# Optimization experiments

Measured on AMD Instinct MI355X. Metric: run time of the kernel, lower is better.

## Reference

```python
import jax, jax.numpy as jnp
import numpy as np

NUM_LAYERS = 2

def setup_inputs() -> dict:
    key = jax.random.key(0)
    ks = jax.random.split(key, 10)
    N, E, V, D, G = 50000, 800000, 100000, 128, 64
    node_ids = jax.random.randint(ks[0], (N,), 0, V)
    edge_index = jax.random.randint(ks[1], (2, E), 0, N)
    batch = jnp.sort(jax.random.randint(ks[2], (N,), 0, G))
    embed = jax.random.normal(ks[3], (V, D), dtype=jnp.float32)
    conv_w = jax.random.normal(ks[4], (NUM_LAYERS, D, D), dtype=jnp.float32) * (1.0 / np.sqrt(D))
    w_ih = jax.random.normal(ks[5], (3 * D, D), dtype=jnp.float32) * (1.0 / np.sqrt(D))
    w_hh = jax.random.normal(ks[6], (3 * D, D), dtype=jnp.float32) * (1.0 / np.sqrt(D))
    b_ih = jax.random.normal(ks[7], (3 * D,), dtype=jnp.float32) * 0.01
    b_hh = jax.random.normal(ks[8], (3 * D,), dtype=jnp.float32) * 0.01
    return {"node_ids": node_ids, "edge_index": edge_index, "batch": batch,
            "num_graphs": 64, "embed": embed, "conv_w": conv_w,
            "w_ih": w_ih, "w_hh": w_hh, "b_ih": b_ih, "b_hh": b_hh}


def _gru_cell(x, h, w_ih, w_hh, b_ih, b_hh):
    # torch.nn.GRUCell math; gate order r, z, n
    gi = x @ w_ih.T + b_ih
    gh = h @ w_hh.T + b_hh
    i_r, i_z, i_n = jnp.split(gi, 3, axis=-1)
    h_r, h_z, h_n = jnp.split(gh, 3, axis=-1)
    r = jax.nn.sigmoid(i_r + h_r)
    z = jax.nn.sigmoid(i_z + h_z)
    n = jnp.tanh(i_n + r * h_n)
    return (1.0 - z) * n + z * h


def reference(node_ids, edge_index, batch, num_graphs, embed, conv_w, w_ih, w_hh, b_ih, b_hh):
    N = node_ids.shape[0]
    src, dst = edge_index[0], edge_index[1]
    h = embed[node_ids]  # [N, D]
    for i in range(NUM_LAYERS):
        m = h @ conv_w[i]                                   # [N, D]
        agg = jax.ops.segment_sum(m[src], dst, num_segments=N)  # scatter-add messages
        h = _gru_cell(agg, h, w_ih, w_hh, b_ih, b_hh)
    # global mean pool per graph
    sums = jax.ops.segment_sum(h, batch, num_segments=num_graphs)       # [G, D]
    counts = jax.ops.segment_sum(jnp.ones((N,), h.dtype), batch, num_segments=num_graphs)
    return sums / jnp.maximum(counts, 1.0)[:, None]
```

## Files before the change

kernel.cpp:

```cpp
#include <hip/hip_runtime.h>
#include <hip/hip_bf16.h>


#define DTHREADS 256
#define BSHIFT 7
#define BNODES 128

typedef __attribute__((ext_vector_type(8))) short bf16x8;
typedef __attribute__((ext_vector_type(4))) float f32x4;

__device__ __forceinline__ float sigf(float x) { return 1.0f / (1.0f + __expf(-x)); }
__device__ __forceinline__ float tanhfast(float x) { return 1.0f - 2.0f / (1.0f + __expf(2.0f * x)); }

__device__ __forceinline__ unsigned short f2bf_rne(float x) {
  unsigned int u = __float_as_uint(x);
  u += 0x7fff + ((u >> 16) & 1);
  return (unsigned short)(u >> 16);
}
__device__ __forceinline__ float bf2f(unsigned int lo16) {
  return __uint_as_float(lo16 << 16);
}

__global__ __launch_bounds__(DTHREADS) void gather_kernel(
    const float* __restrict__ embed, const int* __restrict__ node_ids,
    unsigned short* __restrict__ hb, int N) {
  int idx = blockIdx.x * DTHREADS + threadIdx.x;
  if (idx >= N * 32) return;
  int n = idx >> 5;
  int c = (idx & 31) * 4;
  int v = node_ids[n];
  float4 val = *(const float4*)&embed[(size_t)v * 128 + c];
  unsigned short b[4] = {f2bf_rne(val.x), f2bf_rne(val.y), f2bf_rne(val.z), f2bf_rne(val.w)};
  *(ushort4*)&hb[(size_t)n * 128 + c] = *(ushort4*)b;
}

__global__ __launch_bounds__(DTHREADS) void bucket_hist_kernel(
    const int* __restrict__ dst, int* __restrict__ gcnt, int E, int NB) {
  __shared__ int lc[512];
  int tid = threadIdx.x;
  for (int i = tid; i < NB; i += DTHREADS) lc[i] = 0;
  __syncthreads();
  int base = blockIdx.x * 4096;
  #pragma unroll
  for (int q = 0; q < 16; ++q) {
    int e = base + q * 256 + tid;
    if (e < E) atomicAdd(&lc[dst[e] >> BSHIFT], 1);
  }
  __syncthreads();
  for (int i = tid; i < NB; i += DTHREADS) {
    int c = lc[i];
    if (c) atomicAdd(&gcnt[i], c);
  }
}

__global__ __launch_bounds__(512) void bucket_scan_kernel(
    const int* __restrict__ gcnt, int* __restrict__ ptr, int* __restrict__ cur,
    int* __restrict__ row_ptr, int NB, int N) {
  int tid = threadIdx.x;
  int lane = tid & 63, wv = tid >> 6;
  int v = (tid < NB) ? gcnt[tid] : 0;
  int x = v;
  #pragma unroll
  for (int off = 1; off < 64; off <<= 1) {
    int y = __shfl_up(x, (unsigned)off, 64);
    if (lane >= off) x += y;
  }
  __shared__ int ws[8];
  if (lane == 63) ws[wv] = x;
  __syncthreads();
  int woff = 0;
  for (int w = 0; w < wv; ++w) woff += ws[w];
  int excl = woff + x - v;
  if (tid < NB) { ptr[tid] = excl; cur[tid] = excl; }
  if (tid == 511) { int tot = woff + x; ptr[NB] = tot; row_ptr[N] = tot; }
}

__global__ __launch_bounds__(DTHREADS) void bucket_scatter_kernel(
    const int* __restrict__ src, const int* __restrict__ dst,
    int* __restrict__ cur, unsigned int* __restrict__ ebuf, int E, int NB) {
  __shared__ int lc[512];
  __shared__ int lbs[512];
  int tid = threadIdx.x;
  for (int i = tid; i < NB; i += DTHREADS) lc[i] = 0;
  __syncthreads();
  int base = blockIdx.x * 4096;
  int rank[16];
  #pragma unroll
  for (int q = 0; q < 16; ++q) {
    int e = base + q * 256 + tid;
    if (e < E) rank[q] = atomicAdd(&lc[dst[e] >> BSHIFT], 1);
  }
  __syncthreads();
  for (int i = tid; i < NB; i += DTHREADS) {
    int c = lc[i];
    lbs[i] = c ? atomicAdd(&cur[i], c) : 0;
  }
  __syncthreads();
  #pragma unroll
  for (int q = 0; q < 16; ++q) {
    int e = base + q * 256 + tid;
    if (e < E) {
      int d = dst[e];
      unsigned int pk = (unsigned int)src[e] | ((unsigned int)(d & (BNODES - 1)) << 17);
      ebuf[lbs[d >> BSHIFT] + rank[q]] = pk;
    }
  }
}

__global__ __launch_bounds__(DTHREADS) void bucket_sort_kernel(
    const unsigned int* __restrict__ ebuf, const int* __restrict__ ptr,
    int* __restrict__ row_ptr, int* __restrict__ csr_src, int N) {
  __shared__ int cnt[BNODES];
  __shared__ int sc[BNODES];
  const int tid = threadIdx.x;
  const int b = blockIdx.x;
  const int s = ptr[b], e = ptr[b + 1];
  if (tid < BNODES) cnt[tid] = 0;
  __syncthreads();
  for (int i = s + tid; i < e; i += DTHREADS)
    atomicAdd(&cnt[ebuf[i] >> 17], 1);
  __syncthreads();
  if (tid < BNODES) sc[tid] = cnt[tid];
  __syncthreads();
  #pragma unroll
  for (int off = 1; off < BNODES; off <<= 1) {
    int t = 0;
    if (tid < BNODES && tid >= off) t = sc[tid - off];
    __syncthreads();
    if (tid < BNODES) sc[tid] += t;
    __syncthreads();
  }
  if (tid < BNODES) {
    int excl = sc[tid] - cnt[tid];
    int n = b * BNODES + tid;
    if (n < N) row_ptr[n] = s + excl;
    cnt[tid] = excl;
  }
  __syncthreads();
  for (int i = s + tid; i < e; i += DTHREADS) {
    unsigned int pk = ebuf[i];
    int slot = atomicAdd(&cnt[pk >> 17], 1);
    csr_src[s + slot] = (int)(pk & 0x1FFFFu);
  }
}

__global__ __launch_bounds__(DTHREADS) void pack_w_kernel(
    const float* __restrict__ w, unsigned short* __restrict__ wpk, int J) {
  int f = blockIdx.x * DTHREADS + threadIdx.x;
  if (f >= J * 16) return;
  int l = f & 63;
  int s = (f >> 6) & 3;
  int t = (f >> 8) & 3;
  int jb = f >> 10;
  int j = jb * 64 + t * 16 + (l & 15);
  int kb = s * 32 + (l >> 4) * 8;
  unsigned short o[8];
  #pragma unroll
  for (int i = 0; i < 8; ++i) o[i] = f2bf_rne(w[j * 128 + kb + i]);
  *(uint4*)&wpk[(size_t)f * 8] = *(uint4*)o;
}

__global__ __launch_bounds__(DTHREADS) void pack_wc_kernel(
    const float* __restrict__ conv, const float* __restrict__ w_ih,
    unsigned short* __restrict__ wpk) {
  int id = blockIdx.x * DTHREADS + threadIdx.x;
  if (id >= 384 * 128) return;
  int f = id >> 3, i = id & 7;
  int l = f & 63;
  int s = (f >> 6) & 3;
  int t = (f >> 8) & 3;
  int jb = f >> 10;
  int j = jb * 64 + t * 16 + (l & 15);
  int k = s * 32 + (l >> 4) * 8 + i;
  float acc = 0.f;
  for (int d = 0; d < 128; d += 4) {
    float4 cv = *(const float4*)&conv[k * 128 + d];
    float4 wv = *(const float4*)&w_ih[j * 128 + d];
    acc += cv.x * wv.x + cv.y * wv.y + cv.z * wv.z + cv.w * wv.w;
  }
  wpk[(size_t)f * 8 + i] = f2bf_rne(acc);
}

__global__ __launch_bounds__(DTHREADS) void aggregate_kernel(
    const unsigned short* __restrict__ hb, const int* __restrict__ row_ptr,
    const int* __restrict__ csr_src, unsigned short* __restrict__ agg, int N) {
  int w = (blockIdx.x * DTHREADS + threadIdx.x) >> 6;
  if (w >= N) return;
  int lane = threadIdx.x & 63;
  int g = lane >> 4;
  int c = lane & 15;
  int s = row_ptr[w], e = row_ptr[w + 1];
  float acc[8] = {0.f, 0.f, 0.f, 0.f, 0.f, 0.f, 0.f, 0.f};
  for (int i = s; i < e; i += 8) {
    int iA = i + g, iB = i + g + 4;
    bool vA = iA < e, vB = iB < e;
    int sA = csr_src[vA ? iA : s];
    int sB = csr_src[vB ? iB : s];
    uint4 a = *(const uint4*)&hb[(size_t)sA * 128 + c * 8];
    uint4 b = *(const uint4*)&hb[(size_t)sB * 128 + c * 8];
    const unsigned int* ap = (const unsigned int*)&a;
    const unsigned int* bp = (const unsigned int*)&b;
    if (vA) {
      #pragma unroll
      for (int q = 0; q < 4; ++q) {
        acc[2 * q]     += bf2f(ap[q] & 0xffffu);
        acc[2 * q + 1] += bf2f(ap[q] >> 16);
      }
    }
    if (vB) {
      #pragma unroll
      for (int q = 0; q < 4; ++q) {
        acc[2 * q]     += bf2f(bp[q] & 0xffffu);
        acc[2 * q + 1] += bf2f(bp[q] >> 16);
      }
    }
  }
  #pragma unroll
  for (int q = 0; q < 8; ++q) acc[q] += __shfl_xor(acc[q], 16, 64);
  #pragma unroll
  for (int q = 0; q < 8; ++q) acc[q] += __shfl_xor(acc[q], 32, 64);
  if (g == 0) {
    unsigned int o[4];
    #pragma unroll
    for (int q = 0; q < 4; ++q)
      o[q] = (unsigned int)f2bf_rne(acc[2 * q]) | ((unsigned int)f2bf_rne(acc[2 * q + 1]) << 16);
    *(uint4*)&agg[(size_t)w * 128 + c * 8] = *(uint4*)o;
  }
}

__global__ __launch_bounds__(DTHREADS) void fused_gru_kernel(
    const unsigned short* __restrict__ aggb, const unsigned short* __restrict__ wpk_wc,
    const unsigned short* __restrict__ wpk_hh, const float* __restrict__ b_ih,
    const float* __restrict__ b_hh, unsigned short* __restrict__ hb, int N) {
  __shared__ __align__(16) unsigned short Ag[32 * 128];
  __shared__ __align__(16) unsigned short Hs[32 * 128];
  const int tid = threadIdx.x;
  const int n0 = blockIdx.x * 32;

  #pragma unroll
  for (int it = 0; it < 2; ++it) {
    int c = it * 256 + tid;
    int row = c >> 4, col = c & 15;
    int n = n0 + row;
    uint4 va = make_uint4(0, 0, 0, 0), vh = make_uint4(0, 0, 0, 0);
    if (n < N) {
      va = *(const uint4*)&aggb[(size_t)n * 128 + col * 8];
      vh = *(const uint4*)&hb[(size_t)n * 128 + col * 8];
    }
    int dc = col ^ (row & 15);
    *(uint4*)&Ag[row * 128 + dc * 8] = va;
    *(uint4*)&Hs[row * 128 + dc * 8] = vh;
  }
  __syncthreads();

  const int wv = tid >> 6, lane = tid & 63;
  const int lm = lane & 15, quad = lane >> 4;

  f32x4 accI[2][2][3], accH[2][2][3];
  #pragma unroll
  for (int mi = 0; mi < 2; ++mi)
    #pragma unroll
    for (int u = 0; u < 2; ++u)
      #pragma unroll
      for (int g = 0; g < 3; ++g) {
        accI[mi][u][g] = (f32x4){0.f, 0.f, 0.f, 0.f};
        accH[mi][u][g] = (f32x4){0.f, 0.f, 0.f, 0.f};
      }

  #pragma unroll
  for (int s = 0; s < 4; ++s) {
    bf16x8 afA[2], afH[2];
    #pragma unroll
    for (int mi = 0; mi < 2; ++mi) {
      int m = mi * 16 + lm;
      int chunk = (s * 4 + quad) ^ (m & 15);
      afA[mi] = *(const bf16x8*)&Ag[m * 128 + chunk * 8];
      afH[mi] = *(const bf16x8*)&Hs[m * 128 + chunk * 8];
    }
    #pragma unroll
    for (int g = 0; g < 3; ++g) {
      int jb = g * 2 + (wv >> 1);
      #pragma unroll
      for (int u = 0; u < 2; ++u) {
        int t = (wv & 1) * 2 + u;
        size_t f = ((size_t)(jb * 4 + t) * 4 + s) * 64 + lane;
        bf16x8 bI = *(const bf16x8*)&wpk_wc[f * 8];
        bf16x8 bH = *(const bf16x8*)&wpk_hh[f * 8];
        #pragma unroll
        for (int mi = 0; mi < 2; ++mi) {
          accI[mi][u][g] = __builtin_amdgcn_mfma_f32_16x16x32_bf16(afA[mi], bI, accI[mi][u][g], 0, 0, 0);
          accH[mi][u][g] = __builtin_amdgcn_mfma_f32_16x16x32_bf16(afH[mi], bH, accH[mi][u][g], 0, 0, 0);
        }
      }
    }
  }

  #pragma unroll
  for (int u = 0; u < 2; ++u) {
    int jc = wv * 32 + u * 16 + lm;
    float bir = b_ih[jc], biz = b_ih[128 + jc], bin_ = b_ih[256 + jc];
    float bhr = b_hh[jc], bhz = b_hh[128 + jc], bhn = b_hh[256 + jc];
    int c0 = jc >> 3, ej = jc & 7;
    #pragma unroll
    for (int mi = 0; mi < 2; ++mi) {
      #pragma unroll
      for (int r = 0; r < 4; ++r) {
        int row = mi * 16 + quad * 4 + r;
        int n = n0 + row;
        if (n >= N) continue;
        float ir = accI[mi][u][0][r] + bir;
        float iz = accI[mi][u][1][r] + biz;
        float in_ = accI[mi][u][2][r] + bin_;
        float hr = accH[mi][u][0][r] + bhr;
        float hz = accH[mi][u][1][r] + bhz;
        float hn = accH[mi][u][2][r] + bhn;
        float rr = sigf(ir + hr);
        float zz = sigf(iz + hz);
        float nn = tanhfast(in_ + rr * hn);
        float hold = bf2f((unsigned int)Hs[row * 128 + ((c0 ^ (row & 15)) * 8) + ej]);
        hb[(size_t)n * 128 + jc] = f2bf_rne((1.f - zz) * nn + zz * hold);
      }
    }
  }
}

__global__ __launch_bounds__(DTHREADS) void pool1_kernel(
    const unsigned short* __restrict__ hb, const int* __restrict__ batch,
    float* __restrict__ outsum, int N) {
  int b = blockIdx.x;
  int c = threadIdx.x & 127;
  int half = threadIdx.x >> 7;
  int nbeg = b * 64;
  int nend = min(nbeg + 64, N);
  float acc = 0.f;
  int cur = -1;
  for (int n = nbeg + half; n < nend; n += 2) {
    int g = batch[n];
    if (g != cur) {
      if (cur >= 0) atomicAdd(&outsum[(size_t)cur * 128 + c], acc);
      acc = 0.f;
      cur = g;
    }
    acc += bf2f((unsigned int)hb[(size_t)n * 128 + c]);
  }
  if (cur >= 0) atomicAdd(&outsum[(size_t)cur * 128 + c], acc);
}

__device__ __forceinline__ int lbound(const int* a, int n, int key) {
  int lo = 0, hi = n;
  while (lo < hi) {
    int mid = (lo + hi) >> 1;
    if (a[mid] < key) lo = mid + 1; else hi = mid;
  }
  return lo;
}

__global__ __launch_bounds__(128) void pool2_kernel(
    const float* __restrict__ outsum, const int* __restrict__ batch,
    float* __restrict__ out, int N) {
  int g = blockIdx.x;
  int c = threadIdx.x;
  int lo = lbound(batch, N, g);
  int hi = lbound(batch, N, g + 1);
  out[(size_t)g * 128 + c] = outsum[(size_t)g * 128 + c] / (float)max(hi - lo, 1);
}

extern "C" void kernel_launch(void* const* d_in, const int* in_sizes, int n_in,
                              void* d_out, int out_size, void* d_ws, size_t ws_size,
                              hipStream_t stream) {
  const int* node_ids = (const int*)d_in[0];
  const int* edge_index = (const int*)d_in[1];
  const int* batch = (const int*)d_in[2];
  const float* embed = (const float*)d_in[4];
  const float* conv_w = (const float*)d_in[5];
  const float* w_ih = (const float*)d_in[6];
  const float* w_hh = (const float*)d_in[7];
  const float* b_ih = (const float*)d_in[8];
  const float* b_hh = (const float*)d_in[9];
  float* out = (float*)d_out;

  const int N = in_sizes[0];
  const int E = in_sizes[1] / 2;
  const int G = out_size / 128;
  const int NUM_LAYERS = in_sizes[5] / (128 * 128);
  const int NB = (N + BNODES - 1) >> BSHIFT;

  const int* e_src = edge_index;
  const int* e_dst = edge_index + E;

  char* p = (char*)d_ws;
  unsigned short* hb = (unsigned short*)p;    p += (size_t)N * 128 * 2;
  unsigned short* aggb = (unsigned short*)p;  p += (size_t)N * 128 * 2;
  float* outsum = (float*)p;                  p += (size_t)G * 128 * 4;
  unsigned short* wpk_hh = (unsigned short*)p; p += (size_t)384 * 128 * 2;
  unsigned short* wpk_wc = (unsigned short*)p; p += (size_t)NUM_LAYERS * 384 * 128 * 2;
  int* bkt_cnt = (int*)p;  p += 512 * 4;
  int* bkt_ptr = (int*)p;  p += 513 * 4;
  int* bkt_cur = (int*)p;  p += 512 * 4;
  int* row_ptr = (int*)p;  p += (size_t)(N + 1) * 4;
  unsigned int* ebuf = (unsigned int*)p;  p += (size_t)E * 4;
  int* csr_src = (int*)p;  p += (size_t)E * 4;

  const int nEB = (E + 4095) / 4096;

  hipMemsetAsync(bkt_cnt, 0, 512 * sizeof(int), stream);
  hipMemsetAsync(outsum, 0, (size_t)G * 128 * sizeof(float), stream);

  bucket_hist_kernel<<<nEB, DTHREADS, 0, stream>>>(e_dst, bkt_cnt, E, NB);
  bucket_scan_kernel<<<1, 512, 0, stream>>>(bkt_cnt, bkt_ptr, bkt_cur, row_ptr, NB, N);
  bucket_scatter_kernel<<<nEB, DTHREADS, 0, stream>>>(e_src, e_dst, bkt_cur, ebuf, E, NB);
  bucket_sort_kernel<<<NB, DTHREADS, 0, stream>>>(ebuf, bkt_ptr, row_ptr, csr_src, N);

  pack_w_kernel<<<(384 * 16 + DTHREADS - 1) / DTHREADS, DTHREADS, 0, stream>>>(w_hh, wpk_hh, 384);
  for (int L = 0; L < NUM_LAYERS; ++L)
    pack_wc_kernel<<<(384 * 128 + DTHREADS - 1) / DTHREADS, DTHREADS, 0, stream>>>(
        conv_w + (size_t)L * 128 * 128, w_ih, wpk_wc + (size_t)L * 384 * 128);

  gather_kernel<<<(N * 32 + DTHREADS - 1) / DTHREADS, DTHREADS, 0, stream>>>(embed, node_ids, hb, N);

  const int nb32 = (N + 31) / 32;
  for (int L = 0; L < NUM_LAYERS; ++L) {
    aggregate_kernel<<<((size_t)N * 64 + DTHREADS - 1) / DTHREADS, DTHREADS, 0, stream>>>(
        hb, row_ptr, csr_src, aggb, N);
    fused_gru_kernel<<<nb32, DTHREADS, 0, stream>>>(
        aggb, wpk_wc + (size_t)L * 384 * 128, wpk_hh, b_ih, b_hh, hb, N);
  }

  pool1_kernel<<<(N + 63) / 64, DTHREADS, 0, stream>>>(hb, batch, outsum, N);
  pool2_kernel<<<G, 128, 0, stream>>>(outsum, batch, out, N);
}
```

Before: 327.1 us.

## Make GRU kernel persistent with register-resident weights and prefetched tiles

Turns the fused GRU kernel into a persistent kernel with 256 blocks of 512 threads. Each wave holds its slice of the packed W_ih·conv and W_hh fragments in registers for the whole run instead of reloading them per 32-node tile. The next tile's agg/h rows are prefetched into registers while the current tile is computed, at the cost of an extra barrier and high register pressure. The aggregate kernel is also unrolled to issue four neighbour gathers per lane per iteration instead of two, to raise memory-level parallelism.

```diff
diff --git a/kernel.cpp b/kernel.cpp
--- a/kernel.cpp
+++ b/kernel.cpp
@@ -3,8 +3,6 @@
 
 
 #define DTHREADS 256
-#define BSHIFT 7
-#define BNODES 128
 
 typedef __attribute__((ext_vector_type(8))) short bf16x8;
 typedef __attribute__((ext_vector_type(4))) float f32x4;
@@ -33,6 +31,9 @@
   unsigned short b[4] = {f2bf_rne(val.x), f2bf_rne(val.y), f2bf_rne(val.z), f2bf_rne(val.w)};
   *(ushort4*)&hb[(size_t)n * 128 + c] = *(ushort4*)b;
 }
+
+#define BSHIFT 7
+#define BNODES 128
 
 __global__ __launch_bounds__(DTHREADS) void bucket_hist_kernel(
     const int* __restrict__ dst, int* __restrict__ gcnt, int E, int NB) {
@@ -191,27 +192,26 @@
   int c = lane & 15;
   int s = row_ptr[w], e = row_ptr[w + 1];
   float acc[8] = {0.f, 0.f, 0.f, 0.f, 0.f, 0.f, 0.f, 0.f};
-  for (int i = s; i < e; i += 8) {
-    int iA = i + g, iB = i + g + 4;
-    bool vA = iA < e, vB = iB < e;
-    int sA = csr_src[vA ? iA : s];
-    int sB = csr_src[vB ? iB : s];
-    uint4 a = *(const uint4*)&hb[(size_t)sA * 128 + c * 8];
-    uint4 b = *(const uint4*)&hb[(size_t)sB * 128 + c * 8];
-    const unsigned int* ap = (const unsigned int*)&a;
-    const unsigned int* bp = (const unsigned int*)&b;
-    if (vA) {
-      #pragma unroll
-      for (int q = 0; q < 4; ++q) {
-        acc[2 * q]     += bf2f(ap[q] & 0xffffu);
-        acc[2 * q + 1] += bf2f(ap[q] >> 16);
-      }
-    }
-    if (vB) {
-      #pragma unroll
-      for (int q = 0; q < 4; ++q) {
-        acc[2 * q]     += bf2f(bp[q] & 0xffffu);
-        acc[2 * q + 1] += bf2f(bp[q] >> 16);
+  for (int i = s; i < e; i += 16) {
+    int idx[4]; bool vl[4]; uint4 d[4];
+    #pragma unroll
+    for (int q = 0; q < 4; ++q) {
+      int ii = i + g + q * 4;
+      vl[q] = ii < e;
+      idx[q] = csr_src[vl[q] ? ii : s];
+    }
+    #pragma unroll
+    for (int q = 0; q < 4; ++q)
+      d[q] = *(const uint4*)&hb[(size_t)idx[q] * 128 + c * 8];
+    #pragma unroll
+    for (int q = 0; q < 4; ++q) {
+      if (vl[q]) {
+        const unsigned int* dp = (const unsigned int*)&d[q];
+        #pragma unroll
+        for (int k = 0; k < 4; ++k) {
+          acc[2 * k]     += bf2f(dp[k] & 0xffffu);
+          acc[2 * k + 1] += bf2f(dp[k] >> 16);
+        }
       }
     }
   }
@@ -228,79 +228,92 @@
   }
 }
 
-__global__ __launch_bounds__(DTHREADS) void fused_gru_kernel(
+__global__ __launch_bounds__(512, 2) void fused_gru_kernel(
     const unsigned short* __restrict__ aggb, const unsigned short* __restrict__ wpk_wc,
     const unsigned short* __restrict__ wpk_hh, const float* __restrict__ b_ih,
-    const float* __restrict__ b_hh, unsigned short* __restrict__ hb, int N) {
+    const float* __restrict__ b_hh, unsigned short* __restrict__ hb,
+    int N, int nchunks) {
   __shared__ __align__(16) unsigned short Ag[32 * 128];
   __shared__ __align__(16) unsigned short Hs[32 * 128];
   const int tid = threadIdx.x;
-  const int n0 = blockIdx.x * 32;
-
-  #pragma unroll
-  for (int it = 0; it < 2; ++it) {
-    int c = it * 256 + tid;
-    int row = c >> 4, col = c & 15;
-    int n = n0 + row;
-    uint4 va = make_uint4(0, 0, 0, 0), vh = make_uint4(0, 0, 0, 0);
-    if (n < N) {
-      va = *(const uint4*)&aggb[(size_t)n * 128 + col * 8];
-      vh = *(const uint4*)&hb[(size_t)n * 128 + col * 8];
-    }
-    int dc = col ^ (row & 15);
-    *(uint4*)&Ag[row * 128 + dc * 8] = va;
-    *(uint4*)&Hs[row * 128 + dc * 8] = vh;
-  }
-  __syncthreads();
-
   const int wv = tid >> 6, lane = tid & 63;
   const int lm = lane & 15, quad = lane >> 4;
 
-  f32x4 accI[2][2][3], accH[2][2][3];
-  #pragma unroll
-  for (int mi = 0; mi < 2; ++mi)
-    #pragma unroll
-    for (int u = 0; u < 2; ++u)
+  bf16x8 BI[3][4], BH[3][4];
+  #pragma unroll
+  for (int g = 0; g < 3; ++g) {
+    int jb = g * 2 + (wv >> 2);
+    int t = wv & 3;
+    #pragma unroll
+    for (int s = 0; s < 4; ++s) {
+      size_t f = ((size_t)(jb * 4 + t) * 4 + s) * 64 + lane;
+      BI[g][s] = *(const bf16x8*)&wpk_wc[f * 8];
+      BH[g][s] = *(const bf16x8*)&wpk_hh[f * 8];
+    }
+  }
+
+  const int jc = wv * 16 + lm;
+  const float bir = b_ih[jc], biz = b_ih[128 + jc], bin_ = b_ih[256 + jc];
+  const float bhr = b_hh[jc], bhz = b_hh[128 + jc], bhn = b_hh[256 + jc];
+  const int c0 = jc >> 3, ej = jc & 7;
+
+  const int srow = tid >> 4, scol = tid & 15;
+  const int sdc = (scol ^ (srow & 15)) * 8;
+
+  int ci = blockIdx.x;
+  uint4 va = make_uint4(0, 0, 0, 0), vh = make_uint4(0, 0, 0, 0);
+  if (ci < nchunks) {
+    int n = ci * 32 + srow;
+    if (n < N) {
+      va = *(const uint4*)&aggb[(size_t)n * 128 + scol * 8];
+      vh = *(const uint4*)&hb[(size_t)n * 128 + scol * 8];
+    }
+  }
+
+  for (; ci < nchunks; ci += gridDim.x) {
+    *(uint4*)&Ag[srow * 128 + sdc] = va;
+    *(uint4*)&Hs[srow * 128 + sdc] = vh;
+    __syncthreads();
+
+    int cn = ci + gridDim.x;
+    va = make_uint4(0, 0, 0, 0); vh = make_uint4(0, 0, 0, 0);
+    if (cn < nchunks) {
+      int n = cn * 32 + srow;
+      if (n < N) {
+        va = *(const uint4*)&aggb[(size_t)n * 128 + scol * 8];
+        vh = *(const uint4*)&hb[(size_t)n * 128 + scol * 8];
+      }
+    }
+
+    f32x4 accI[2][3], accH[2][3];
+    #pragma unroll
+    for (int mi = 0; mi < 2; ++mi)
       #pragma unroll
       for (int g = 0; g < 3; ++g) {
-        accI[mi][u][g] = (f32x4){0.f, 0.f, 0.f, 0.f};
-        accH[mi][u][g] = (f32x4){0.f, 0.f, 0.f, 0.f};
+        accI[mi][g] = (f32x4){0.f, 0.f, 0.f, 0.f};
+        accH[mi][g] = (f32x4){0.f, 0.f, 0.f, 0.f};
       }
 
-  #pragma unroll
-  for (int s = 0; s < 4; ++s) {
-    bf16x8 afA[2], afH[2];
-    #pragma unroll
-    for (int mi = 0; mi < 2; ++mi) {
-      int m = mi * 16 + lm;
-      int chunk = (s * 4 + quad) ^ (m & 15);
-      afA[mi] = *(const bf16x8*)&Ag[m * 128 + chunk * 8];
-      afH[mi] = *(const bf16x8*)&Hs[m * 128 + chunk * 8];
-    }
-    #pragma unroll
-    for (int g = 0; g < 3; ++g) {
-      int jb = g * 2 + (wv >> 1);
+    #pragma unroll
+    for (int s = 0; s < 4; ++s) {
+      bf16x8 afA[2], afH[2];
       #pragma unroll
-      for (int u = 0; u < 2; ++u) {
-        int t = (wv & 1) * 2 + u;
-        size_t f = ((size_t)(jb * 4 + t) * 4 + s) * 64 + lane;
-        bf16x8 bI = *(const bf16x8*)&wpk_wc[f * 8];
-        bf16x8 bH = *(const bf16x8*)&wpk_hh[f * 8];
+      for (int mi = 0; mi < 2; ++mi) {
+        int m = mi * 16 + lm;
+        int chunk = (s * 4 + quad) ^ (m & 15);
+        afA[mi] = *(const bf16x8*)&Ag[m * 128 + chunk * 8];
+        afH[mi] = *(const bf16x8*)&Hs[m * 128 + chunk * 8];
+      }
+      #pragma unroll
+      for (int g = 0; g < 3; ++g)
         #pragma unroll
         for (int mi = 0; mi < 2; ++mi) {
-          accI[mi][u][g] = __builtin_amdgcn_mfma_f32_16x16x32_bf16(afA[mi], bI, accI[mi][u][g], 0, 0, 0);
-          accH[mi][u][g] = __builtin_amdgcn_mfma_f32_16x16x32_bf16(afH[mi], bH, accH[mi][u][g], 0, 0, 0);
+          accI[mi][g] = __builtin_amdgcn_mfma_f32_16x16x32_bf16(afA[mi], BI[g][s], accI[mi][g], 0, 0, 0);
+          accH[mi][g] = __builtin_amdgcn_mfma_f32_16x16x32_bf16(afH[mi], BH[g][s], accH[mi][g], 0, 0, 0);
         }
-      }
-    }
-  }
-
-  #pragma unroll
-  for (int u = 0; u < 2; ++u) {
-    int jc = wv * 32 + u * 16 + lm;
-    float bir = b_ih[jc], biz = b_ih[128 + jc], bin_ = b_ih[256 + jc];
-    float bhr = b_hh[jc], bhz = b_hh[128 + jc], bhn = b_hh[256 + jc];
-    int c0 = jc >> 3, ej = jc & 7;
+    }
+
+    const int n0 = ci * 32;
     #pragma unroll
     for (int mi = 0; mi < 2; ++mi) {
       #pragma unroll
@@ -308,12 +321,12 @@
         int row = mi * 16 + quad * 4 + r;
         int n = n0 + row;
         if (n >= N) continue;
-        float ir = accI[mi][u][0][r] + bir;
-        float iz = accI[mi][u][1][r] + biz;
-        float in_ = accI[mi][u][2][r] + bin_;
-        float hr = accH[mi][u][0][r] + bhr;
-        float hz = accH[mi][u][1][r] + bhz;
-        float hn = accH[mi][u][2][r] + bhn;
+        float ir = accI[mi][0][r] + bir;
+        float iz = accI[mi][1][r] + biz;
+        float in_ = accI[mi][2][r] + bin_;
+        float hr = accH[mi][0][r] + bhr;
+        float hz = accH[mi][1][r] + bhz;
+        float hn = accH[mi][2][r] + bhn;
         float rr = sigf(ir + hr);
         float zz = sigf(iz + hz);
         float nn = tanhfast(in_ + rr * hn);
@@ -321,6 +334,7 @@
         hb[(size_t)n * 128 + jc] = f2bf_rne((1.f - zz) * nn + zz * hold);
       }
     }
+    __syncthreads();
   }
 }
 
@@ -418,12 +432,12 @@
 
   gather_kernel<<<(N * 32 + DTHREADS - 1) / DTHREADS, DTHREADS, 0, stream>>>(embed, node_ids, hb, N);
 
-  const int nb32 = (N + 31) / 32;
+  const int nchunks = (N + 31) / 32;
   for (int L = 0; L < NUM_LAYERS; ++L) {
     aggregate_kernel<<<((size_t)N * 64 + DTHREADS - 1) / DTHREADS, DTHREADS, 0, stream>>>(
         hb, row_ptr, csr_src, aggb, N);
-    fused_gru_kernel<<<nb32, DTHREADS, 0, stream>>>(
-        aggb, wpk_wc + (size_t)L * 384 * 128, wpk_hh, b_ih, b_hh, hb, N);
+    fused_gru_kernel<<<256, 512, 0, stream>>>(
+        aggb, wpk_wc + (size_t)L * 384 * 128, wpk_hh, b_ih, b_hh, hb, N, nchunks);
   }
 
   pool1_kernel<<<(N + 63) / 64, DTHREADS, 0, stream>>>(hb, batch, outsum, N);
```

After: 296.5 us. 1.1x faster.
